# Optimization experiments

Hardware: AMD Instinct MI355X
Metric: run time of the kernel (lower is better)

The kernel has to match this reference:

```python
import jax, jax.numpy as jnp
import numpy as np

D_MODEL = 1024
NEG_BIG = -1e9  # matches TF float32 branch


def setup_inputs() -> dict:
    key = jax.random.key(0)
    kq, kk, kv, km = jax.random.split(key, 4)
    B, S, D = 4, 2048, D_MODEL
    q = jax.random.normal(kq, (B, S, D), dtype=jnp.float32)
    k = jax.random.normal(kk, (B, S, D), dtype=jnp.float32)
    v = jax.random.normal(kv, (B, S, D), dtype=jnp.float32)
    mask = jax.random.randint(km, (B, 1, S), 0, 2, dtype=jnp.int32)  # 1 = masked
    return {"q": q, "k": k, "v": v, "mask": mask}


def reference(q, k, v, mask):
    scale = jnp.asarray(D_MODEL, q.dtype) ** -0.5
    # [B,S,S] attention logits
    logits = jnp.einsum("bqd,bkd->bqk", q, k) * scale
    logits = logits + mask.astype(q.dtype) * NEG_BIG
    weights = jax.nn.softmax(logits, axis=-1)
    return jnp.einsum("bqk,bkd->bqd", weights, v)
```

## Files before the change

kernel.cpp:

```cpp
#include <hip/hip_runtime.h>
#include <hip/hip_bf16.h>
#include <cstdint>

#define B_    4
#define S_    2048
#define D_    1024
#define SCALE 0.03125f
#define NEG_BIG -1e9f

typedef __attribute__((ext_vector_type(8))) short short8;
typedef __attribute__((ext_vector_type(4))) float f32x4;

__device__ __forceinline__ ushort f2bf(float f) {
  uint32_t u = __float_as_uint(f);
  u += 0x7fffu + ((u >> 16) & 1u);
  return (ushort)(u >> 16);
}

__device__ __forceinline__ void load16_to_lds(const void* g, void* l) {
  __builtin_amdgcn_global_load_lds(
      (const __attribute__((address_space(1))) uint32_t*)g,
      (__attribute__((address_space(3))) uint32_t*)l, 16, 0, 0);
}

__global__ void convert_bf16(const float* __restrict__ X, ushort* __restrict__ Xb) {
  size_t i = ((size_t)blockIdx.x * 256 + threadIdx.x) * 8;
  float4 a = *(const float4*)(X + i);
  float4 c = *(const float4*)(X + i + 4);
  uint4 w;
  w.x = (uint)f2bf(a.x) | ((uint)f2bf(a.y) << 16);
  w.y = (uint)f2bf(a.z) | ((uint)f2bf(a.w) << 16);
  w.z = (uint)f2bf(c.x) | ((uint)f2bf(c.y) << 16);
  w.w = (uint)f2bf(c.z) | ((uint)f2bf(c.w) << 16);
  *(uint4*)(Xb + i) = w;
}

__global__ void transpose_v(const float* __restrict__ V, ushort* __restrict__ Vt) {
  __shared__ ushort tile[64][68];
  int tx = threadIdx.x & 15, ty = threadIdx.x >> 4;
  int s0 = blockIdx.x * 64, d0 = blockIdx.y * 64, b = blockIdx.z;
  const float* src = V + ((size_t)b * S_ + s0) * D_ + d0;
  for (int i = 0; i < 4; ++i) {
    int row = ty + i * 16;
    float4 a = *(const float4*)(src + (size_t)row * D_ + tx * 4);
    ushort4 w;
    w.x = f2bf(a.x); w.y = f2bf(a.y); w.z = f2bf(a.z); w.w = f2bf(a.w);
    *(ushort4*)&tile[row][tx * 4] = w;
  }
  __syncthreads();
  ushort* dst = Vt + ((size_t)b * D_ + d0) * S_ + s0;
  for (int i = 0; i < 4; ++i) {
    int drow = ty + i * 16;
    ushort4 w;
    w.x = tile[tx * 4 + 0][drow];
    w.y = tile[tx * 4 + 1][drow];
    w.z = tile[tx * 4 + 2][drow];
    w.w = tile[tx * 4 + 3][drow];
    *(ushort4*)(dst + (size_t)drow * S_ + tx * 4) = w;
  }
}

template<int KDIM, int LDA, int LDB, int LDC,
         long long BATCHA, long long BATCHB, long long BATCHC, int EPI>
__global__ void gemm_bt(const ushort* __restrict__ A, const ushort* __restrict__ Bt,
                        float* __restrict__ C, const int* __restrict__ mask) {
  __shared__ __align__(16) ushort As[128 * 32];
  __shared__ __align__(16) ushort Bs[128 * 32];

  int tid  = threadIdx.x;
  int lane = tid & 63;
  int wave = tid >> 6;
  int bn = blockIdx.x, bm = blockIdx.y, b = blockIdx.z;
  int l16 = lane & 15, quad = lane >> 4;
  int wm = (wave & 1) * 64, wn = (wave >> 1) * 64;

  const ushort* Ab = A  + (size_t)b * BATCHA + (size_t)(bm * 128) * LDA;
  const ushort* Bb = Bt + (size_t)b * BATCHB + (size_t)(bn * 128) * LDB;

  f32x4 acc[4][4];
#pragma unroll
  for (int i = 0; i < 4; ++i)
#pragma unroll
    for (int j = 0; j < 4; ++j) acc[i][j] = (f32x4){0.f, 0.f, 0.f, 0.f};

  for (int kc = 0; kc < KDIM / 32; ++kc) {
    __syncthreads();
#pragma unroll
    for (int h = 0; h < 2; ++h) {
      int c = tid + h * 256;
      const ushort* ga = Ab + (size_t)(c >> 2) * LDA + kc * 32 + (c & 3) * 8;
      const ushort* gb = Bb + (size_t)(c >> 2) * LDB + kc * 32 + (c & 3) * 8;
      load16_to_lds(ga, As + c * 8);
      load16_to_lds(gb, Bs + c * 8);
    }
    __syncthreads();

    short8 af[4], bf[4];
#pragma unroll
    for (int mt = 0; mt < 4; ++mt)
      af[mt] = *(const short8*)(As + (wm + mt * 16 + l16) * 32 + quad * 8);
#pragma unroll
    for (int nt = 0; nt < 4; ++nt)
      bf[nt] = *(const short8*)(Bs + (wn + nt * 16 + l16) * 32 + quad * 8);
#pragma unroll
    for (int mt = 0; mt < 4; ++mt)
#pragma unroll
      for (int nt = 0; nt < 4; ++nt)
        acc[mt][nt] = __builtin_amdgcn_mfma_f32_16x16x32_bf16(af[mt], bf[nt], acc[mt][nt], 0, 0, 0);
  }

  float* Cb = C + (size_t)b * BATCHC + (size_t)(bm * 128) * LDC + bn * 128;
#pragma unroll
  for (int nt = 0; nt < 4; ++nt) {
    int col = wn + nt * 16 + l16;
    float madd = 0.f;
    if (EPI == 0) madd = mask[b * S_ + bn * 128 + col] ? NEG_BIG : 0.f;
#pragma unroll
    for (int mt = 0; mt < 4; ++mt)
#pragma unroll
      for (int r = 0; r < 4; ++r) {
        int row = wm + mt * 16 + quad * 4 + r;
        float v = acc[mt][nt][r];
        if (EPI == 0) v = v * SCALE + madd;
        Cb[(size_t)row * LDC + col] = v;
      }
  }
}

__global__ void softmax_rows(const float* __restrict__ S, ushort* __restrict__ P) {
  int q = blockIdx.x, b = blockIdx.y;
  int tid = threadIdx.x, wave = tid >> 6, lane = tid & 63;
  const float* row = S + ((size_t)b * S_ + q) * S_;

  float4 x0 = *(const float4*)(row + tid * 8);
  float4 x1 = *(const float4*)(row + tid * 8 + 4);
  float x[8] = {x0.x, x0.y, x0.z, x0.w, x1.x, x1.y, x1.z, x1.w};

  float m = x[0];
#pragma unroll
  for (int i = 1; i < 8; ++i) m = fmaxf(m, x[i]);
  for (int off = 1; off <= 32; off <<= 1) m = fmaxf(m, __shfl_xor(m, off));
  __shared__ float redm[4], reds[4];
  if (lane == 0) redm[wave] = m;
  __syncthreads();
  m = fmaxf(fmaxf(redm[0], redm[1]), fmaxf(redm[2], redm[3]));

  float e[8], s = 0.f;
#pragma unroll
  for (int i = 0; i < 8; ++i) { e[i] = __expf(x[i] - m); s += e[i]; }
  for (int off = 1; off <= 32; off <<= 1) s += __shfl_xor(s, off);
  if (lane == 0) reds[wave] = s;
  __syncthreads();
  s = reds[0] + reds[1] + reds[2] + reds[3];
  float rinv = 1.0f / s;

  uint4 w;
  w.x = (uint)f2bf(e[0] * rinv) | ((uint)f2bf(e[1] * rinv) << 16);
  w.y = (uint)f2bf(e[2] * rinv) | ((uint)f2bf(e[3] * rinv) << 16);
  w.z = (uint)f2bf(e[4] * rinv) | ((uint)f2bf(e[5] * rinv) << 16);
  w.w = (uint)f2bf(e[6] * rinv) | ((uint)f2bf(e[7] * rinv) << 16);
  *(uint4*)(P + ((size_t)b * S_ + q) * S_ + tid * 8) = w;
}

extern "C" void kernel_launch(void* const* d_in, const int* in_sizes, int n_in,
                              void* d_out, int out_size, void* d_ws, size_t ws_size,
                              hipStream_t stream) {
  const float* Q   = (const float*)d_in[0];
  const float* K   = (const float*)d_in[1];
  const float* V   = (const float*)d_in[2];
  const int*  mask = (const int*)d_in[3];
  float* Out = (float*)d_out;

  const size_t E = (size_t)B_ * S_ * D_;
  ushort* Qb = (ushort*)d_ws;
  ushort* Kb = Qb + E;
  ushort* Vt = Kb + E;
  float*  Sb = (float*)(Vt + E);
  ushort* P  = Qb;

  convert_bf16<<<4096, 256, 0, stream>>>(Q, Qb);
  convert_bf16<<<4096, 256, 0, stream>>>(K, Kb);
  transpose_v<<<dim3(32, 16, 4), 256, 0, stream>>>(V, Vt);

  gemm_bt<1024, 1024, 1024, 2048,
          (long long)2048 * 1024, (long long)2048 * 1024, (long long)2048 * 2048, 0>
      <<<dim3(16, 16, 4), 256, 0, stream>>>(Qb, Kb, Sb, mask);

  softmax_rows<<<dim3(2048, 4), 256, 0, stream>>>(Sb, P);

  gemm_bt<2048, 2048, 2048, 1024,
          (long long)2048 * 2048, (long long)1024 * 2048, (long long)2048 * 1024, 1>
      <<<dim3(8, 16, 4), 256, 0, stream>>>(P, Vt, Out, nullptr);
}
```

Measured before the change: 262.3 us.

## Remap GEMM blocks per XCD, fuse prep kernels, use wave-per-row softmax

Merges the Q/K bf16 conversion and V transpose into a single prep launch. Remaps GEMM block indices so each XCD works on one batch half with a serpentine tile order, aiming for better L2 reuse of A/B tiles. Softmax now processes one row per wave with shuffle-only reductions, dropping LDS and block barriers. The block mapping assumes round-robin dispatch across 8 XCDs, which is hardware-scheduling dependent.

```diff
diff --git a/kernel.cpp b/kernel.cpp
--- a/kernel.cpp
+++ b/kernel.cpp
@@ -23,22 +23,29 @@
       (__attribute__((address_space(3))) uint32_t*)l, 16, 0, 0);
 }
 
-__global__ void convert_bf16(const float* __restrict__ X, ushort* __restrict__ Xb) {
-  size_t i = ((size_t)blockIdx.x * 256 + threadIdx.x) * 8;
-  float4 a = *(const float4*)(X + i);
-  float4 c = *(const float4*)(X + i + 4);
-  uint4 w;
-  w.x = (uint)f2bf(a.x) | ((uint)f2bf(a.y) << 16);
-  w.y = (uint)f2bf(a.z) | ((uint)f2bf(a.w) << 16);
-  w.z = (uint)f2bf(c.x) | ((uint)f2bf(c.y) << 16);
-  w.w = (uint)f2bf(c.z) | ((uint)f2bf(c.w) << 16);
-  *(uint4*)(Xb + i) = w;
-}
-
-__global__ void transpose_v(const float* __restrict__ V, ushort* __restrict__ Vt) {
+__global__ void prep(const float* __restrict__ Q, const float* __restrict__ K,
+                     const float* __restrict__ V, ushort* __restrict__ Qb,
+                     ushort* __restrict__ Kb, ushort* __restrict__ Vt) {
   __shared__ ushort tile[64][68];
+  int id = blockIdx.x;
+  if (id < 8192) {
+    const float* X = (id < 4096) ? Q : K;
+    ushort* Xb     = (id < 4096) ? Qb : Kb;
+    int cid = id & 4095;
+    size_t i = ((size_t)cid * 256 + threadIdx.x) * 8;
+    float4 a = *(const float4*)(X + i);
+    float4 c = *(const float4*)(X + i + 4);
+    uint4 w;
+    w.x = (uint)f2bf(a.x) | ((uint)f2bf(a.y) << 16);
+    w.y = (uint)f2bf(a.z) | ((uint)f2bf(a.w) << 16);
+    w.z = (uint)f2bf(c.x) | ((uint)f2bf(c.y) << 16);
+    w.w = (uint)f2bf(c.z) | ((uint)f2bf(c.w) << 16);
+    *(uint4*)(Xb + i) = w;
+    return;
+  }
+  int t = id - 8192;
+  int s0 = (t & 31) * 64, d0 = ((t >> 5) & 15) * 64, b = t >> 9;
   int tx = threadIdx.x & 15, ty = threadIdx.x >> 4;
-  int s0 = blockIdx.x * 64, d0 = blockIdx.y * 64, b = blockIdx.z;
   const float* src = V + ((size_t)b * S_ + s0) * D_ + d0;
   for (int i = 0; i < 4; ++i) {
     int row = ty + i * 16;
@@ -67,10 +74,24 @@
   __shared__ __align__(16) ushort As[128 * 32];
   __shared__ __align__(16) ushort Bs[128 * 32];
 
+  int linear = blockIdx.x;
+  int xcd = linear & 7, idx = linear >> 3;
+  int b = xcd >> 1, half = xcd & 1;
+  int bm, bn;
+  if (EPI == 0) {
+    bm = idx >> 3;
+    int s = idx & 7;
+    bn = half * 8 + ((bm & 1) ? 7 - s : s);
+  } else {
+    int bmh = idx >> 3;
+    bm = half * 8 + bmh;
+    int s = idx & 7;
+    bn = (bmh & 1) ? 7 - s : s;
+  }
+
   int tid  = threadIdx.x;
   int lane = tid & 63;
   int wave = tid >> 6;
-  int bn = blockIdx.x, bm = blockIdx.y, b = blockIdx.z;
   int l16 = lane & 15, quad = lane >> 4;
   int wm = (wave & 1) * 64, wn = (wave >> 1) * 64;
 
@@ -128,38 +149,37 @@
 }
 
 __global__ void softmax_rows(const float* __restrict__ S, ushort* __restrict__ P) {
-  int q = blockIdx.x, b = blockIdx.y;
-  int tid = threadIdx.x, wave = tid >> 6, lane = tid & 63;
-  const float* row = S + ((size_t)b * S_ + q) * S_;
-
-  float4 x0 = *(const float4*)(row + tid * 8);
-  float4 x1 = *(const float4*)(row + tid * 8 + 4);
-  float x[8] = {x0.x, x0.y, x0.z, x0.w, x1.x, x1.y, x1.z, x1.w};
-
+  int row = blockIdx.x * 4 + (threadIdx.x >> 6);
+  int lane = threadIdx.x & 63;
+  const float* src = S + (size_t)row * S_;
+
+  float x[32];
+#pragma unroll
+  for (int j = 0; j < 8; ++j) {
+    float4 v = *(const float4*)(src + lane * 4 + j * 256);
+    x[j * 4 + 0] = v.x; x[j * 4 + 1] = v.y; x[j * 4 + 2] = v.z; x[j * 4 + 3] = v.w;
+  }
   float m = x[0];
 #pragma unroll
-  for (int i = 1; i < 8; ++i) m = fmaxf(m, x[i]);
-  for (int off = 1; off <= 32; off <<= 1) m = fmaxf(m, __shfl_xor(m, off));
-  __shared__ float redm[4], reds[4];
-  if (lane == 0) redm[wave] = m;
-  __syncthreads();
-  m = fmaxf(fmaxf(redm[0], redm[1]), fmaxf(redm[2], redm[3]));
-
-  float e[8], s = 0.f;
-#pragma unroll
-  for (int i = 0; i < 8; ++i) { e[i] = __expf(x[i] - m); s += e[i]; }
-  for (int off = 1; off <= 32; off <<= 1) s += __shfl_xor(s, off);
-  if (lane == 0) reds[wave] = s;
-  __syncthreads();
-  s = reds[0] + reds[1] + reds[2] + reds[3];
+  for (int i = 1; i < 32; ++i) m = fmaxf(m, x[i]);
+  for (int off = 1; off < 64; off <<= 1) m = fmaxf(m, __shfl_xor(m, off));
+
+  float e[32], s = 0.f;
+#pragma unroll
+  for (int i = 0; i < 32; ++i) { e[i] = __expf(x[i] - m); s += e[i]; }
+  for (int off = 1; off < 64; off <<= 1) s += __shfl_xor(s, off);
   float rinv = 1.0f / s;
 
-  uint4 w;
-  w.x = (uint)f2bf(e[0] * rinv) | ((uint)f2bf(e[1] * rinv) << 16);
-  w.y = (uint)f2bf(e[2] * rinv) | ((uint)f2bf(e[3] * rinv) << 16);
-  w.z = (uint)f2bf(e[4] * rinv) | ((uint)f2bf(e[5] * rinv) << 16);
-  w.w = (uint)f2bf(e[6] * rinv) | ((uint)f2bf(e[7] * rinv) << 16);
-  *(uint4*)(P + ((size_t)b * S_ + q) * S_ + tid * 8) = w;
+  ushort* dst = P + (size_t)row * S_;
+#pragma unroll
+  for (int j = 0; j < 8; ++j) {
+    ushort4 w;
+    w.x = f2bf(e[j * 4 + 0] * rinv);
+    w.y = f2bf(e[j * 4 + 1] * rinv);
+    w.z = f2bf(e[j * 4 + 2] * rinv);
+    w.w = f2bf(e[j * 4 + 3] * rinv);
+    *(ushort4*)(dst + lane * 4 + j * 256) = w;
+  }
 }
 
 extern "C" void kernel_launch(void* const* d_in, const int* in_sizes, int n_in,
@@ -178,17 +198,15 @@
   float*  Sb = (float*)(Vt + E);
   ushort* P  = Qb;
 
-  convert_bf16<<<4096, 256, 0, stream>>>(Q, Qb);
-  convert_bf16<<<4096, 256, 0, stream>>>(K, Kb);
-  transpose_v<<<dim3(32, 16, 4), 256, 0, stream>>>(V, Vt);
+  prep<<<10240, 256, 0, stream>>>(Q, K, V, Qb, Kb, Vt);
 
   gemm_bt<1024, 1024, 1024, 2048,
           (long long)2048 * 1024, (long long)2048 * 1024, (long long)2048 * 2048, 0>
-      <<<dim3(16, 16, 4), 256, 0, stream>>>(Qb, Kb, Sb, mask);
-
-  softmax_rows<<<dim3(2048, 4), 256, 0, stream>>>(Sb, P);
+      <<<1024, 256, 0, stream>>>(Qb, Kb, Sb, mask);
+
+  softmax_rows<<<2048, 256, 0, stream>>>(Sb, P);
 
   gemm_bt<2048, 2048, 2048, 1024,
           (long long)2048 * 2048, (long long)1024 * 2048, (long long)2048 * 1024, 1>
-      <<<dim3(8, 16, 4), 256, 0, stream>>>(P, Vt, Out, nullptr);
-}
+      <<<512, 256, 0, stream>>>(P, Vt, Out, nullptr);
+}
```

New measurement: 244.6 us. 6.8% less time.
